# Kernel tuning notes

Hardware: AMD Instinct MI355X
Metric: run time of the kernel (lower is better)

The kernel has to match this reference:

```python
import jax, jax.numpy as jnp
import numpy as np

LN_EPS = 1e-5  # torch nn.LayerNorm default


def setup_inputs() -> dict:
    key = jax.random.key(0)
    ks = jax.random.split(key, 5)
    B, N, K, H, D = 1, 16384, 16, 4, 32
    q = jax.random.normal(ks[0], (B, N, H, D), dtype=jnp.float32)
    k_neigh = jax.random.normal(ks[1], (B, N, K, H, D), dtype=jnp.float32)
    v_neigh = jax.random.normal(ks[2], (B, N, K, H, D), dtype=jnp.float32)
    geo_f = jax.random.normal(ks[3], (B, N, K, D), dtype=jnp.float32)
    W = jax.random.normal(ks[4], (D, D), dtype=jnp.float32) * (1.0 / np.sqrt(D))
    b = jnp.zeros((D,), dtype=jnp.float32)
    ln_gamma = jnp.ones((D,), dtype=jnp.float32)
    ln_beta = jnp.zeros((D,), dtype=jnp.float32)
    return {"q": q, "k_neigh": k_neigh, "v_neigh": v_neigh, "geo_f": geo_f,
            "W": W, "b": b, "ln_gamma": ln_gamma, "ln_beta": ln_beta}


def reference(q, k_neigh, v_neigh, geo_f, W, b, ln_gamma, ln_beta):
    # q: [B,N,H,D], k_neigh/v_neigh: [B,N,K,H,D], geo_f: [B,N,K,D]
    scale = q.shape[-1] ** (-0.5)
    # broadcasted edge tensor [B,N,K,H,D]
    w = (q[:, :, None, :, :] - k_neigh + geo_f[:, :, :, None, :]) / scale
    # Linear(hdim,hdim) + ReLU + LayerNorm(hdim)
    w = jnp.einsum('bnkhd,ed->bnkhe', w, W) + b
    w = jax.nn.relu(w)
    mu = jnp.mean(w, axis=-1, keepdims=True)
    var = jnp.mean(jnp.square(w - mu), axis=-1, keepdims=True)
    w = (w - mu) * jax.lax.rsqrt(var + LN_EPS) * ln_gamma + ln_beta
    # subtract detached per-neighbor max (shift-invariant for softmax)
    w = w - jax.lax.stop_gradient(jnp.max(w, axis=2, keepdims=True))
    attn = jax.nn.softmax(w, axis=2)  # softmax over K neighbors
    # dropout p=0.0 -> identity
    out = jnp.sum(attn * v_neigh, axis=2)  # [B,N,H,D]
    return out
```

## Files before the change

### kernel.cpp

```cpp
#include <hip/hip_runtime.h>
#include <hip/hip_bf16.h>

constexpr int KNB = 16;
constexpr int HH  = 4;
constexpr int DD  = 32;
constexpr int WPB   = 4;
constexpr int ITERS = 4;

typedef __attribute__((ext_vector_type(4))) float f32x4;
typedef __attribute__((ext_vector_type(8))) short bf16x8;
union BFRAG { bf16x8 v; unsigned u[4]; };

__device__ __forceinline__ unsigned pk_bf16(float a, float b) {
    union { __hip_bfloat162 b2; unsigned u; } r;
    r.b2 = __float22bfloat162_rn(make_float2(a, b));
    return r.u;
}
__device__ __forceinline__ float2 unpk_bf16(unsigned u) {
    union { unsigned u; __hip_bfloat162 b2; } r; r.u = u;
    return make_float2(__bfloat162float(r.b2.x), __bfloat162float(r.b2.y));
}

template<bool GUARD>
__global__ __launch_bounds__(256) void geoneigh_mfma3(
    const float* __restrict__ q, const float* __restrict__ kn,
    const float* __restrict__ vn, const float* __restrict__ geo,
    const float* __restrict__ W, const float* __restrict__ bvec,
    const float* __restrict__ gamma, const float* __restrict__ beta,
    float* __restrict__ out, int nUnits, int strideW)
{
    const int l   = threadIdx.x & 63;
    const int gw0 = __builtin_amdgcn_readfirstlane(
                        blockIdx.x * WPB + (threadIdx.x >> 6));

    const int lm = l & 15;
    const int lg = l >> 4;

    const float SC = 5.656854249492381f;

    BFRAG Wh[2], Wl[2];
    #pragma unroll
    for (int t = 0; t < 2; ++t) {
        const float* wr = &W[(t * 16 + lm) * DD + lg * 8];
        const float4 wa = *(const float4*)wr;
        const float4 wb = *(const float4*)(wr + 4);
        float wf[8] = {wa.x * SC, wa.y * SC, wa.z * SC, wa.w * SC,
                       wb.x * SC, wb.y * SC, wb.z * SC, wb.w * SC};
        #pragma unroll
        for (int p = 0; p < 4; ++p) {
            const unsigned h = pk_bf16(wf[2 * p], wf[2 * p + 1]);
            const float2 hr = unpk_bf16(h);
            Wh[t].u[p] = h;
            Wl[t].u[p] = pk_bf16(wf[2 * p] - hr.x, wf[2 * p + 1] - hr.y);
        }
    }
    float bias[2], gam[2], bet[2];
    #pragma unroll
    for (int t = 0; t < 2; ++t) {
        bias[t] = bvec[lm + 16 * t];
        gam[t]  = gamma[lm + 16 * t];
        bet[t]  = beta[lm + 16 * t];
    }

    const int koff = lm * (HH * DD) + lg * 8;
    const int goff = lm * DD + lg * 8;
    const int qoff = lg * 8;
    const int voff = (lg * 4) * (HH * DD) + lm;

    #pragma unroll
    for (int it = 0; it < ITERS; ++it) {
        const int gwi = gw0 + it * strideW;
        if (GUARD && gwi >= nUnits) break;
        const int n  = gwi >> 1;
        const int h0 = (gwi & 1) * 2;
        const size_t nb = (size_t)n;

        const float* kb = kn  + nb * (KNB * HH * DD) + h0 * DD + koff;
        const float* gb = geo + nb * (KNB * DD) + goff;
        const float* qb = q   + nb * (HH * DD) + h0 * DD + qoff;
        const float* vb = vn  + nb * (KNB * HH * DD) + h0 * DD + voff;

        const float4 gf0 = *(const float4*)gb;
        const float4 gf1 = *(const float4*)(gb + 4);
        float4 kf[2][2], qf[2][2];
        #pragma unroll
        for (int u = 0; u < 2; ++u) {
            kf[u][0] = *(const float4*)(kb + u * DD);
            kf[u][1] = *(const float4*)(kb + u * DD + 4);
            qf[u][0] = *(const float4*)(qb + u * DD);
            qf[u][1] = *(const float4*)(qb + u * DD + 4);
        }
        float vreg[2][2][4];
        #pragma unroll
        for (int u = 0; u < 2; ++u)
            #pragma unroll
            for (int t = 0; t < 2; ++t)
                #pragma unroll
                for (int r = 0; r < 4; ++r)
                    vreg[u][t][r] = vb[r * (HH * DD) + u * DD + 16 * t];

        f32x4 acc[2][2];
        #pragma unroll
        for (int u = 0; u < 2; ++u) {
            float wv[8];
            #pragma unroll
            for (int p = 0; p < 2; ++p) {
                const float4 kq = kf[u][p], qq = qf[u][p];
                const float4 gg = p ? gf1 : gf0;
                wv[4 * p + 0] = qq.x - kq.x + gg.x;
                wv[4 * p + 1] = qq.y - kq.y + gg.y;
                wv[4 * p + 2] = qq.z - kq.z + gg.z;
                wv[4 * p + 3] = qq.w - kq.w + gg.w;
            }
            BFRAG Ah, Al;
            #pragma unroll
            for (int p = 0; p < 4; ++p) {
                const unsigned h = pk_bf16(wv[2 * p], wv[2 * p + 1]);
                const float2 hr = unpk_bf16(h);
                Ah.u[p] = h;
                Al.u[p] = pk_bf16(wv[2 * p] - hr.x, wv[2 * p + 1] - hr.y);
            }
            #pragma unroll
            for (int t = 0; t < 2; ++t) {
                f32x4 c = {bias[t], bias[t], bias[t], bias[t]};
                c = __builtin_amdgcn_mfma_f32_16x16x32_bf16(Ah.v, Wh[t].v, c, 0, 0, 0);
                c = __builtin_amdgcn_mfma_f32_16x16x32_bf16(Ah.v, Wl[t].v, c, 0, 0, 0);
                c = __builtin_amdgcn_mfma_f32_16x16x32_bf16(Al.v, Wh[t].v, c, 0, 0, 0);
                acc[u][t] = c;
            }
        }

        float outv[2], sumv[2];
        #pragma unroll
        for (int u = 0; u < 2; ++u) {
            float x[2][4], t1[4], t2[4];
            #pragma unroll
            for (int t = 0; t < 2; ++t)
                #pragma unroll
                for (int r = 0; r < 4; ++r)
                    x[t][r] = fmaxf(acc[u][t][r], 0.f);
            #pragma unroll
            for (int r = 0; r < 4; ++r) {
                t1[r] = x[0][r] + x[1][r];
                t2[r] = x[0][r] * x[0][r] + x[1][r] * x[1][r];
            }
            #pragma unroll
            for (int m = 1; m <= 8; m <<= 1) {
                #pragma unroll
                for (int r = 0; r < 4; ++r) {
                    t1[r] += __shfl_xor(t1[r], m);
                    t2[r] += __shfl_xor(t2[r], m);
                }
            }
            float z[2][4];
            #pragma unroll
            for (int r = 0; r < 4; ++r) {
                const float mu  = t1[r] * 0.03125f;
                const float var = fmaxf(t2[r] * 0.03125f - mu * mu, 0.f);
                const float inv = rsqrtf(var + 1e-5f);
                #pragma unroll
                for (int t = 0; t < 2; ++t)
                    z[t][r] = (x[t][r] - mu) * inv * gam[t] + bet[t];
            }
            float S[2], o[2];
            #pragma unroll
            for (int t = 0; t < 2; ++t) {
                float s = 0.f, oo = 0.f;
                #pragma unroll
                for (int r = 0; r < 4; ++r) {
                    const float p = __expf(z[t][r]);
                    s += p;
                    oo = fmaf(p, vreg[u][t][r], oo);
                }
                s  += __shfl_xor(s, 16);
                s  += __shfl_xor(s, 32);
                oo += __shfl_xor(oo, 16);
                oo += __shfl_xor(oo, 32);
                S[t] = s; o[t] = oo;
            }
            const int sel = lg & 1;
            outv[u] = sel ? o[1] : o[0];
            sumv[u] = sel ? S[1] : S[0];
        }

        const int us = l >> 5;
        const float oo = us ? outv[1] : outv[0];
        const float ss = us ? sumv[1] : sumv[0];
        out[(nb * HH + h0 + us) * DD + (l & 31)] = __fdividef(oo, ss);
    }
}

extern "C" void kernel_launch(void* const* d_in, const int* in_sizes, int n_in,
                              void* d_out, int out_size, void* d_ws, size_t ws_size,
                              hipStream_t stream) {
    const float* q   = (const float*)d_in[0];
    const float* kn  = (const float*)d_in[1];
    const float* vn  = (const float*)d_in[2];
    const float* geo = (const float*)d_in[3];
    const float* W   = (const float*)d_in[4];
    const float* b   = (const float*)d_in[5];
    const float* gam = (const float*)d_in[6];
    const float* bet = (const float*)d_in[7];
    float* out = (float*)d_out;

    const int BN      = in_sizes[0] / (HH * DD);
    const int nUnits  = BN * 2;
    const int blocks  = (nUnits + WPB * ITERS - 1) / (WPB * ITERS);
    const int strideW = blocks * WPB;
    const bool exact  = (nUnits == blocks * WPB * ITERS);

    if (exact)
        hipLaunchKernelGGL(geoneigh_mfma3<false>, dim3(blocks), dim3(256), 0,
                           stream, q, kn, vn, geo, W, b, gam, bet, out,
                           nUnits, strideW);
    else
        hipLaunchKernelGGL(geoneigh_mfma3<true>, dim3(blocks), dim3(256), 0,
                           stream, q, kn, vn, geo, W, b, gam, bet, out,
                           nUnits, strideW);
}
```

Measured before the change: 63.75 us.

## Process all four heads per wave to reuse geo loads and batch memory

Each wave now handles a whole point (all four heads) instead of half a point, so the geo_f slice is loaded once per point rather than twice. All k, q and v loads for the point are issued up front behind a sched_barrier to raise memory-level parallelism. Iterations per wave drop to two and launch bounds now request four blocks per SM. Softmax switches to exp2 with log2e folded into gamma and beta. The extra live registers for four heads' worth of loads may strain occupancy against the launch-bounds target.

```diff
diff --git a/kernel.cpp b/kernel.cpp
--- a/kernel.cpp
+++ b/kernel.cpp
@@ -5,7 +5,7 @@
 constexpr int HH  = 4;
 constexpr int DD  = 32;
 constexpr int WPB   = 4;
-constexpr int ITERS = 4;
+constexpr int ITERS = 2;
 
 typedef __attribute__((ext_vector_type(4))) float f32x4;
 typedef __attribute__((ext_vector_type(8))) short bf16x8;
@@ -22,12 +22,12 @@
 }
 
 template<bool GUARD>
-__global__ __launch_bounds__(256) void geoneigh_mfma3(
+__global__ __launch_bounds__(256, 4) void geoneigh_mfma5(
     const float* __restrict__ q, const float* __restrict__ kn,
     const float* __restrict__ vn, const float* __restrict__ geo,
     const float* __restrict__ W, const float* __restrict__ bvec,
     const float* __restrict__ gamma, const float* __restrict__ beta,
-    float* __restrict__ out, int nUnits, int strideW)
+    float* __restrict__ out, int nN, int strideN)
 {
     const int l   = threadIdx.x & 63;
     const int gw0 = __builtin_amdgcn_readfirstlane(
@@ -36,7 +36,8 @@
     const int lm = l & 15;
     const int lg = l >> 4;
 
-    const float SC = 5.656854249492381f;
+    const float SC    = 5.656854249492381f;
+    const float LOG2E = 1.4426950408889634f;
 
     BFRAG Wh[2], Wl[2];
     #pragma unroll
@@ -54,12 +55,12 @@
             Wl[t].u[p] = pk_bf16(wf[2 * p] - hr.x, wf[2 * p + 1] - hr.y);
         }
     }
-    float bias[2], gam[2], bet[2];
+    float bias[2], gamL[2], betL[2];
     #pragma unroll
     for (int t = 0; t < 2; ++t) {
         bias[t] = bvec[lm + 16 * t];
-        gam[t]  = gamma[lm + 16 * t];
-        bet[t]  = beta[lm + 16 * t];
+        gamL[t] = gamma[lm + 16 * t] * LOG2E;
+        betL[t] = beta[lm + 16 * t] * LOG2E;
     }
 
     const int koff = lm * (HH * DD) + lg * 8;
@@ -69,124 +70,128 @@
 
     #pragma unroll
     for (int it = 0; it < ITERS; ++it) {
-        const int gwi = gw0 + it * strideW;
-        if (GUARD && gwi >= nUnits) break;
-        const int n  = gwi >> 1;
-        const int h0 = (gwi & 1) * 2;
+        const int n = gw0 + it * strideN;
+        if (GUARD && n >= nN) break;
         const size_t nb = (size_t)n;
 
-        const float* kb = kn  + nb * (KNB * HH * DD) + h0 * DD + koff;
         const float* gb = geo + nb * (KNB * DD) + goff;
-        const float* qb = q   + nb * (HH * DD) + h0 * DD + qoff;
-        const float* vb = vn  + nb * (KNB * HH * DD) + h0 * DD + voff;
+        const float* kb = kn  + nb * (KNB * HH * DD) + koff;
+        const float* qb = q   + nb * (HH * DD) + qoff;
+        const float* vb = vn  + nb * (KNB * HH * DD) + voff;
 
         const float4 gf0 = *(const float4*)gb;
         const float4 gf1 = *(const float4*)(gb + 4);
-        float4 kf[2][2], qf[2][2];
-        #pragma unroll
-        for (int u = 0; u < 2; ++u) {
-            kf[u][0] = *(const float4*)(kb + u * DD);
-            kf[u][1] = *(const float4*)(kb + u * DD + 4);
-            qf[u][0] = *(const float4*)(qb + u * DD);
-            qf[u][1] = *(const float4*)(qb + u * DD + 4);
+        float4 kf[4][2], qf[4][2];
+        #pragma unroll
+        for (int h = 0; h < 4; ++h) {
+            kf[h][0] = *(const float4*)(kb + h * DD);
+            kf[h][1] = *(const float4*)(kb + h * DD + 4);
+            qf[h][0] = *(const float4*)(qb + h * DD);
+            qf[h][1] = *(const float4*)(qb + h * DD + 4);
         }
-        float vreg[2][2][4];
-        #pragma unroll
-        for (int u = 0; u < 2; ++u)
+        float vr[4][2][4];
+        #pragma unroll
+        for (int h = 0; h < 4; ++h)
             #pragma unroll
             for (int t = 0; t < 2; ++t)
                 #pragma unroll
                 for (int r = 0; r < 4; ++r)
-                    vreg[u][t][r] = vb[r * (HH * DD) + u * DD + 16 * t];
-
-        f32x4 acc[2][2];
-        #pragma unroll
-        for (int u = 0; u < 2; ++u) {
-            float wv[8];
+                    vr[h][t][r] = vb[r * (HH * DD) + h * DD + 16 * t];
+        __builtin_amdgcn_sched_barrier(0);
+
+        #pragma unroll
+        for (int hp = 0; hp < 2; ++hp) {
+            f32x4 acc[2][2];
             #pragma unroll
-            for (int p = 0; p < 2; ++p) {
-                const float4 kq = kf[u][p], qq = qf[u][p];
-                const float4 gg = p ? gf1 : gf0;
-                wv[4 * p + 0] = qq.x - kq.x + gg.x;
-                wv[4 * p + 1] = qq.y - kq.y + gg.y;
-                wv[4 * p + 2] = qq.z - kq.z + gg.z;
-                wv[4 * p + 3] = qq.w - kq.w + gg.w;
+            for (int u = 0; u < 2; ++u) {
+                const int h = hp * 2 + u;
+                float wv[8];
+                #pragma unroll
+                for (int p = 0; p < 2; ++p) {
+                    const float4 kq = kf[h][p], qq = qf[h][p];
+                    const float4 gg = p ? gf1 : gf0;
+                    wv[4 * p + 0] = qq.x - kq.x + gg.x;
+                    wv[4 * p + 1] = qq.y - kq.y + gg.y;
+                    wv[4 * p + 2] = qq.z - kq.z + gg.z;
+                    wv[4 * p + 3] = qq.w - kq.w + gg.w;
+                }
+                BFRAG Ah, Al;
+                #pragma unroll
+                for (int p = 0; p < 4; ++p) {
+                    const unsigned hh = pk_bf16(wv[2 * p], wv[2 * p + 1]);
+                    const float2 hr = unpk_bf16(hh);
+                    Ah.u[p] = hh;
+                    Al.u[p] = pk_bf16(wv[2 * p] - hr.x, wv[2 * p + 1] - hr.y);
+                }
+                #pragma unroll
+                for (int t = 0; t < 2; ++t) {
+                    f32x4 c = {bias[t], bias[t], bias[t], bias[t]};
+                    c = __builtin_amdgcn_mfma_f32_16x16x32_bf16(Ah.v, Wh[t].v, c, 0, 0, 0);
+                    c = __builtin_amdgcn_mfma_f32_16x16x32_bf16(Ah.v, Wl[t].v, c, 0, 0, 0);
+                    c = __builtin_amdgcn_mfma_f32_16x16x32_bf16(Al.v, Wh[t].v, c, 0, 0, 0);
+                    acc[u][t] = c;
+                }
             }
-            BFRAG Ah, Al;
+
+            float outv[2], sumv[2];
             #pragma unroll
-            for (int p = 0; p < 4; ++p) {
-                const unsigned h = pk_bf16(wv[2 * p], wv[2 * p + 1]);
-                const float2 hr = unpk_bf16(h);
-                Ah.u[p] = h;
-                Al.u[p] = pk_bf16(wv[2 * p] - hr.x, wv[2 * p + 1] - hr.y);
+            for (int u = 0; u < 2; ++u) {
+                const int h = hp * 2 + u;
+                float x[2][4], t1[4], t2[4];
+                #pragma unroll
+                for (int t = 0; t < 2; ++t)
+                    #pragma unroll
+                    for (int r = 0; r < 4; ++r)
+                        x[t][r] = fmaxf(acc[u][t][r], 0.f);
+                #pragma unroll
+                for (int r = 0; r < 4; ++r) {
+                    t1[r] = x[0][r] + x[1][r];
+                    t2[r] = x[0][r] * x[0][r] + x[1][r] * x[1][r];
+                }
+                #pragma unroll
+                for (int m = 1; m <= 8; m <<= 1) {
+                    #pragma unroll
+                    for (int r = 0; r < 4; ++r) {
+                        t1[r] += __shfl_xor(t1[r], m);
+                        t2[r] += __shfl_xor(t2[r], m);
+                    }
+                }
+                float z[2][4];
+                #pragma unroll
+                for (int r = 0; r < 4; ++r) {
+                    const float mu  = t1[r] * 0.03125f;
+                    const float var = fmaxf(t2[r] * 0.03125f - mu * mu, 0.f);
+                    const float inv = rsqrtf(var + 1e-5f);
+                    #pragma unroll
+                    for (int t = 0; t < 2; ++t)
+                        z[t][r] = (x[t][r] - mu) * inv * gamL[t] + betL[t];
+                }
+                float S[2], o[2];
+                #pragma unroll
+                for (int t = 0; t < 2; ++t) {
+                    float s = 0.f, oo = 0.f;
+                    #pragma unroll
+                    for (int r = 0; r < 4; ++r) {
+                        const float p = exp2f(z[t][r]);
+                        s += p;
+                        oo = fmaf(p, vr[h][t][r], oo);
+                    }
+                    s  += __shfl_xor(s, 16);
+                    s  += __shfl_xor(s, 32);
+                    oo += __shfl_xor(oo, 16);
+                    oo += __shfl_xor(oo, 32);
+                    S[t] = s; o[t] = oo;
+                }
+                const int sel = lg & 1;
+                outv[u] = sel ? o[1] : o[0];
+                sumv[u] = sel ? S[1] : S[0];
             }
-            #pragma unroll
-            for (int t = 0; t < 2; ++t) {
-                f32x4 c = {bias[t], bias[t], bias[t], bias[t]};
-                c = __builtin_amdgcn_mfma_f32_16x16x32_bf16(Ah.v, Wh[t].v, c, 0, 0, 0);
-                c = __builtin_amdgcn_mfma_f32_16x16x32_bf16(Ah.v, Wl[t].v, c, 0, 0, 0);
-                c = __builtin_amdgcn_mfma_f32_16x16x32_bf16(Al.v, Wh[t].v, c, 0, 0, 0);
-                acc[u][t] = c;
-            }
+
+            const int us = l >> 5;
+            const float oo = us ? outv[1] : outv[0];
+            const float ss = us ? sumv[1] : sumv[0];
+            out[(nb * HH + hp * 2 + us) * DD + (l & 31)] = __fdividef(oo, ss);
         }
-
-        float outv[2], sumv[2];
-        #pragma unroll
-        for (int u = 0; u < 2; ++u) {
-            float x[2][4], t1[4], t2[4];
-            #pragma unroll
-            for (int t = 0; t < 2; ++t)
-                #pragma unroll
-                for (int r = 0; r < 4; ++r)
-                    x[t][r] = fmaxf(acc[u][t][r], 0.f);
-            #pragma unroll
-            for (int r = 0; r < 4; ++r) {
-                t1[r] = x[0][r] + x[1][r];
-                t2[r] = x[0][r] * x[0][r] + x[1][r] * x[1][r];
-            }
-            #pragma unroll
-            for (int m = 1; m <= 8; m <<= 1) {
-                #pragma unroll
-                for (int r = 0; r < 4; ++r) {
-                    t1[r] += __shfl_xor(t1[r], m);
-                    t2[r] += __shfl_xor(t2[r], m);
-                }
-            }
-            float z[2][4];
-            #pragma unroll
-            for (int r = 0; r < 4; ++r) {
-                const float mu  = t1[r] * 0.03125f;
-                const float var = fmaxf(t2[r] * 0.03125f - mu * mu, 0.f);
-                const float inv = rsqrtf(var + 1e-5f);
-                #pragma unroll
-                for (int t = 0; t < 2; ++t)
-                    z[t][r] = (x[t][r] - mu) * inv * gam[t] + bet[t];
-            }
-            float S[2], o[2];
-            #pragma unroll
-            for (int t = 0; t < 2; ++t) {
-                float s = 0.f, oo = 0.f;
-                #pragma unroll
-                for (int r = 0; r < 4; ++r) {
-                    const float p = __expf(z[t][r]);
-                    s += p;
-                    oo = fmaf(p, vreg[u][t][r], oo);
-                }
-                s  += __shfl_xor(s, 16);
-                s  += __shfl_xor(s, 32);
-                oo += __shfl_xor(oo, 16);
-                oo += __shfl_xor(oo, 32);
-                S[t] = s; o[t] = oo;
-            }
-            const int sel = lg & 1;
-            outv[u] = sel ? o[1] : o[0];
-            sumv[u] = sel ? S[1] : S[0];
-        }
-
-        const int us = l >> 5;
-        const float oo = us ? outv[1] : outv[0];
-        const float ss = us ? sumv[1] : sumv[0];
-        out[(nb * HH + h0 + us) * DD + (l & 31)] = __fdividef(oo, ss);
     }
 }
 
@@ -204,17 +209,16 @@
     float* out = (float*)d_out;
 
     const int BN      = in_sizes[0] / (HH * DD);
-    const int nUnits  = BN * 2;
-    const int blocks  = (nUnits + WPB * ITERS - 1) / (WPB * ITERS);
-    const int strideW = blocks * WPB;
-    const bool exact  = (nUnits == blocks * WPB * ITERS);
+    const int blocks  = (BN + WPB * ITERS - 1) / (WPB * ITERS);
+    const int strideN = blocks * WPB;
+    const bool exact  = (BN == blocks * WPB * ITERS);
 
     if (exact)
-        hipLaunchKernelGGL(geoneigh_mfma3<false>, dim3(blocks), dim3(256), 0,
+        hipLaunchKernelGGL(geoneigh_mfma5<false>, dim3(blocks), dim3(256), 0,
                            stream, q, kn, vn, geo, W, b, gam, bet, out,
-                           nUnits, strideW);
+                           BN, strideN);
     else
-        hipLaunchKernelGGL(geoneigh_mfma3<true>, dim3(blocks), dim3(256), 0,
+        hipLaunchKernelGGL(geoneigh_mfma5<true>, dim3(blocks), dim3(256), 0,
                            stream, q, kn, vn, geo, W, b, gam, bet, out,
-                           nUnits, strideW);
-}
+                           BN, strideN);
+}
```

Result: faster. 62.24 us (-2.4%).
